# Optimization experiments

Hardware: AMD Instinct MI355X
Metric: run time of the kernel (lower is better)

Reference implementation:

```python
import jax, jax.numpy as jnp
import numpy as np

TOP_K = 2

def setup_inputs() -> dict:
    key = jax.random.key(0)
    k1, k2, k3, k4 = jax.random.split(key, 4)
    B, S, H, E, F = 2, 1024, 1024, 16, 1024
    hidden_states = jax.random.normal(k1, (B, S, H), dtype=jnp.float32)
    router_w = jax.random.normal(k2, (H, E), dtype=jnp.float32) * 0.02
    w_gate_up = jax.random.normal(k3, (E, H, 2 * F), dtype=jnp.float32) * 0.02
    w_down = jax.random.normal(k4, (E, F, H), dtype=jnp.float32) * 0.02
    return {"hidden_states": hidden_states, "router_w": router_w,
            "w_gate_up": w_gate_up, "w_down": w_down}

def reference(hidden_states, router_w, w_gate_up, w_down):
    B, S, H = hidden_states.shape
    E = router_w.shape[-1]
    flat = hidden_states.reshape(-1, H)                      # [T, H]
    T = flat.shape[0]
    # Routing: topk_then_softmax (default softmax_order)
    logits = flat @ router_w                                 # [T, E]
    top_vals, top_idx = jax.lax.top_k(logits, TOP_K)         # [T, K]
    routing_weights = jax.nn.softmax(top_vals, axis=-1)      # [T, K]
    # Scatter routing weights into a dense combine matrix [T, E]
    combine = jnp.zeros((T, E), dtype=flat.dtype)
    combine = combine.at[jnp.arange(T)[:, None], top_idx].add(routing_weights)
    # Fused expert FFN (per _FusedExpertTemplate, act_fn = SiLU-gated)
    gu = jnp.einsum('th,ehf->etf', flat, w_gate_up)          # [E, T, 2F]
    gate, up = jnp.split(gu, 2, axis=-1)
    gated = jax.nn.silu(gate) * up                           # [E, T, F]
    expert_out = jnp.einsum('etf,efh->eth', gated, w_down)   # [E, T, H]
    out = jnp.einsum('eth,te->th', expert_out, combine)      # [T, H]
    return out.reshape(B, S, H)
```

## Files before the change

kernel.cpp:

```cpp
#include <hip/hip_runtime.h>

#define T_TOK 2048
#define H_DIM 1024
#define E_NUM 16
#define F_DIM 1024
#define NKB 32

typedef unsigned short u16;
typedef unsigned int u32;
typedef short s16x8 __attribute__((ext_vector_type(8)));
typedef float f32x4 __attribute__((ext_vector_type(4)));

__device__ __forceinline__ float b2f(u16 v) { return __uint_as_float(((u32)v) << 16); }
__device__ __forceinline__ u16 f2b(float f) {
  u32 u = __float_as_uint(f);
  return (u16)((u + 0x7fffu + ((u >> 16) & 1u)) >> 16);
}

__device__ __forceinline__ void gl_lds16(const u32* g, u32* l) {
  __builtin_amdgcn_global_load_lds((const __attribute__((address_space(1))) void*)g,
                                   (__attribute__((address_space(3))) void*)l, 16, 0, 0);
}

__global__ __launch_bounds__(256) void rw_transpose_kernel(const float* __restrict__ rw,
                                                           float* __restrict__ rwT) {
  int idx = blockIdx.x * 256 + threadIdx.x;
  float v = rw[idx];
  rwT[(idx & 15) * 1024 + (idx >> 4)] = v;
}

__global__ __launch_bounds__(256) void router_kernel(const float* __restrict__ hidden,
                                                     const float* __restrict__ rwT,
                                                     int* __restrict__ counts,
                                                     int* __restrict__ routing_e,
                                                     float* __restrict__ routing_w) {
  int wv = threadIdx.x >> 6, lane = threadIdx.x & 63;
  int t = blockIdx.x * 4 + wv;
  const float* xrow = hidden + (size_t)t * H_DIM;
  float acc[E_NUM];
#pragma unroll
  for (int e = 0; e < E_NUM; ++e) acc[e] = 0.f;
  for (int j = 0; j < H_DIM / 64; ++j) {
    int h = j * 64 + lane;
    float x = xrow[h];
#pragma unroll
    for (int e = 0; e < E_NUM; ++e) acc[e] += x * rwT[e * 1024 + h];
  }
#pragma unroll
  for (int e = 0; e < E_NUM; ++e) {
    acc[e] += __shfl_xor(acc[e], 32, 64);
    acc[e] += __shfl_xor(acc[e], 16, 64);
    acc[e] += __shfl_xor(acc[e], 8, 64);
    acc[e] += __shfl_xor(acc[e], 4, 64);
    acc[e] += __shfl_xor(acc[e], 2, 64);
    acc[e] += __shfl_xor(acc[e], 1, 64);
  }
  if (lane == 0) {
    float v0 = -1e30f, v1 = -1e30f;
    int i0 = 0, i1 = 0;
#pragma unroll
    for (int e = 0; e < E_NUM; ++e) {
      float v = acc[e];
      if (v > v0) { v1 = v0; i1 = i0; v0 = v; i0 = e; }
      else if (v > v1) { v1 = v; i1 = e; }
    }
    float p0 = 1.f / (1.f + __expf(v1 - v0));
    routing_e[2 * t] = i0;
    routing_e[2 * t + 1] = i1;
    routing_w[2 * t] = p0;
    routing_w[2 * t + 1] = 1.f - p0;
    atomicAdd(&counts[i0], 1);
    atomicAdd(&counts[i1], 1);
  }
}

__global__ void scatter_kernel(const int* __restrict__ counts, int* __restrict__ offsets,
                               const int* __restrict__ routing_e, const float* __restrict__ routing_w,
                               int* __restrict__ token_of_slot, float* __restrict__ slot_w) {
  __shared__ int offs[E_NUM];
  __shared__ int cur[E_NUM];
  int tid = threadIdx.x;
  if (tid == 0) {
    int s = 0;
    for (int e = 0; e < E_NUM; ++e) { offs[e] = s; s += counts[e]; }
  }
  __syncthreads();
  if (tid < E_NUM) { offsets[tid] = offs[tid]; cur[tid] = offs[tid]; }
  __syncthreads();
  for (int i = tid; i < 2 * T_TOK; i += 256) {
    int e = routing_e[i];
    int pos = atomicAdd(&cur[e], 1);
    token_of_slot[pos] = i >> 1;
    slot_w[pos] = routing_w[i];
  }
}

__device__ __forceinline__ void split_pack(const float* __restrict__ p, uint4& hh, uint4& ll) {
  u16 h[8], l[8];
#pragma unroll
  for (int i = 0; i < 8; ++i) {
    h[i] = f2b(p[i]);
    l[i] = f2b(p[i] - b2f(h[i]));
  }
  hh.x = (u32)h[0] | ((u32)h[1] << 16);
  hh.y = (u32)h[2] | ((u32)h[3] << 16);
  hh.z = (u32)h[4] | ((u32)h[5] << 16);
  hh.w = (u32)h[6] | ((u32)h[7] << 16);
  ll.x = (u32)l[0] | ((u32)l[1] << 16);
  ll.y = (u32)l[2] | ((u32)l[3] << 16);
  ll.z = (u32)l[4] | ((u32)l[5] << 16);
  ll.w = (u32)l[6] | ((u32)l[7] << 16);
}

__global__ __launch_bounds__(256) void prep_x(const float* __restrict__ x, u16* __restrict__ xh,
                                              u16* __restrict__ xl) {
  int i = blockIdx.x * 256 + threadIdx.x;
  float4 a = ((const float4*)x)[2 * i];
  float4 b = ((const float4*)x)[2 * i + 1];
  float v[8] = {a.x, a.y, a.z, a.w, b.x, b.y, b.z, b.w};
  uint4 hh, ll;
  split_pack(v, hh, ll);
  ((uint4*)xh)[i] = hh;
  ((uint4*)xl)[i] = ll;
}

__global__ __launch_bounds__(256) void prep_w(const float* __restrict__ w, u32* __restrict__ wt,
                                              int N) {
  const int e = blockIdx.z, nbk = blockIdx.y, kb = blockIdx.x;
  const float* src = w + (size_t)e * 1024 * N + (size_t)kb * 32 * N + nbk * 128;
  u32* dst = wt + (((size_t)e * gridDim.y + nbk) * NKB + kb) * 2048;
  const int t = threadIdx.x;
  const int n = t & 127, h = t >> 7;
  const int s = ((n >> 3) ^ n) & 3;
  const float* col = src + (size_t)(16 * h) * N + n;
  float v[16];
#pragma unroll
  for (int kk = 0; kk < 16; ++kk) v[kk] = col[(size_t)kk * N];
  __align__(16) u32 wbuf[8];
#pragma unroll
  for (int j = 0; j < 8; ++j) wbuf[j] = (u32)f2b(v[2 * j]) | ((u32)f2b(v[2 * j + 1]) << 16);
  u32* row = dst + n * 16;
  *(uint4*)(row + (((2 * h) ^ s) & 3) * 4) = *(uint4*)&wbuf[0];
  *(uint4*)(row + (((2 * h + 1) ^ s) & 3) * 4) = *(uint4*)&wbuf[4];
}

__device__ __forceinline__ s16x8 read_bfrag(const u32* __restrict__ B, int n, int q) {
  return *(const s16x8*)&B[n * 16 + (((q ^ (n >> 3) ^ n) & 3) << 2)];
}

#define MFMA(a, b, c) __builtin_amdgcn_mfma_f32_16x16x32_bf16(a, b, c, 0, 0, 0)

__global__ __launch_bounds__(256, 2) void moe_gemm1(
    const u16* __restrict__ Xh, const u16* __restrict__ Xl, const u32* __restrict__ wgu_t,
    const int* __restrict__ token_of_slot, const int* __restrict__ counts,
    const int* __restrict__ offsets, u16* __restrict__ act_h, u16* __restrict__ act_l) {
  const int e = blockIdx.z;
  const int cnt = counts[e];
  const int m0 = blockIdx.y * 64;
  if (m0 >= cnt) return;
  const int off = offsets[e];
  const int xb = blockIdx.x;

  __shared__ u32 Bg[4][2048];
  __shared__ u32 Bu[4][2048];

  const int tid = threadIdx.x;
  const int lane = tid & 63;
  const int wv = tid >> 6;
  const int q = lane >> 4, ln = lane & 15;
  const int mb = (wv & 1) * 32, nb = (wv >> 1) * 64;

  const int r0 = m0 + mb + ln, r1 = r0 + 16;
  const int t0 = (r0 < cnt) ? token_of_slot[off + r0] : 0;
  const int t1 = (r1 < cnt) ? token_of_slot[off + r1] : 0;
  const u16* xh0 = Xh + (size_t)t0 * H_DIM + q * 8;
  const u16* xh1 = Xh + (size_t)t1 * H_DIM + q * 8;
  const u16* xl0 = Xl + (size_t)t0 * H_DIM + q * 8;
  const u16* xl1 = Xl + (size_t)t1 * H_DIM + q * 8;

  const u32* g_g = wgu_t + (((size_t)e * 16 + xb) * NKB) * 2048 + tid * 4;
  const u32* g_u = wgu_t + (((size_t)e * 16 + xb + 8) * NKB) * 2048 + tid * 4;

  f32x4 zero = {0.f, 0.f, 0.f, 0.f};
  f32x4 accg[2][4], accu[2][4];
#pragma unroll
  for (int i = 0; i < 2; ++i)
#pragma unroll
    for (int j = 0; j < 4; ++j) { accg[i][j] = zero; accu[i][j] = zero; }

#define G1STAGE(KBN)                                      \
  {                                                       \
    const int bix = (KBN) & 3;                            \
    const u32* sg = g_g + (size_t)(KBN) * 2048;           \
    const u32* su = g_u + (size_t)(KBN) * 2048;           \
    gl_lds16(sg, &Bg[bix][0] + wv * 256);                 \
    gl_lds16(sg + 1024, &Bg[bix][0] + 1024 + wv * 256);   \
    gl_lds16(su, &Bu[bix][0] + wv * 256);                 \
    gl_lds16(su + 1024, &Bu[bix][0] + 1024 + wv * 256);   \
  }

  s16x8 pH0, pH1, pL0, pL1, qH0, qH1, qL0, qL1;

  G1STAGE(0);
  pH0 = *(const s16x8*)(xh0);
  pH1 = *(const s16x8*)(xh1);
  pL0 = *(const s16x8*)(xl0);
  pL1 = *(const s16x8*)(xl1);
  G1STAGE(1);
  G1STAGE(2);

#define G1BODY(KB, H0, H1, L0, L1, NH0, NH1, NL0, NL1, WN, DOPF, DOST)  \
  {                                                                     \
    if (DOPF) {                                                         \
      const int ko = ((KB) + 1) * 32;                                   \
      NH0 = *(const s16x8*)(xh0 + ko);                                  \
      NH1 = *(const s16x8*)(xh1 + ko);                                  \
      NL0 = *(const s16x8*)(xl0 + ko);                                  \
      NL1 = *(const s16x8*)(xl1 + ko);                                  \
    }                                                                   \
    asm volatile("s_waitcnt vmcnt(" WN ")" ::: "memory");               \
    __builtin_amdgcn_sched_barrier(0);                                  \
    __builtin_amdgcn_s_barrier();                                       \
    __builtin_amdgcn_sched_barrier(0);                                  \
    if (DOST) G1STAGE((KB) + 3);                                        \
    const u32* Bgc = &Bg[(KB) & 3][0];                                  \
    const u32* Buc = &Bu[(KB) & 3][0];                                  \
    __builtin_amdgcn_s_setprio(1);                                      \
    _Pragma("unroll") for (int j = 0; j < 4; ++j) {                     \
      s16x8 bg = read_bfrag(Bgc, nb + j * 16 + ln, q);                  \
      s16x8 bu = read_bfrag(Buc, nb + j * 16 + ln, q);                  \
      accg[0][j] = MFMA(H0, bg, accg[0][j]);                            \
      accg[1][j] = MFMA(H1, bg, accg[1][j]);                            \
      accu[0][j] = MFMA(H0, bu, accu[0][j]);                            \
      accu[1][j] = MFMA(H1, bu, accu[1][j]);                            \
      accg[0][j] = MFMA(L0, bg, accg[0][j]);                            \
      accg[1][j] = MFMA(L1, bg, accg[1][j]);                            \
      accu[0][j] = MFMA(L0, bu, accu[0][j]);                            \
      accu[1][j] = MFMA(L1, bu, accu[1][j]);                            \
    }                                                                   \
    __builtin_amdgcn_s_setprio(0);                                      \
  }

  for (int kb = 0; kb < 28; kb += 2) {
    G1BODY(kb, pH0, pH1, pL0, pL1, qH0, qH1, qL0, qL1, "8", 1, 1);
    G1BODY(kb + 1, qH0, qH1, qL0, qL1, pH0, pH1, pL0, pL1, "8", 1, 1);
  }
  G1BODY(28, pH0, pH1, pL0, pL1, qH0, qH1, qL0, qL1, "8", 1, 1);
  G1BODY(29, qH0, qH1, qL0, qL1, pH0, pH1, pL0, pL1, "8", 1, 0);
  G1BODY(30, pH0, pH1, pL0, pL1, qH0, qH1, qL0, qL1, "4", 1, 0);
  G1BODY(31, qH0, qH1, qL0, qL1, pH0, pH1, pL0, pL1, "0", 0, 0);

  const int bcol = xb * 128 + nb + ln;
#pragma unroll
  for (int i = 0; i < 2; ++i) {
#pragma unroll
    for (int r = 0; r < 4; ++r) {
      int row = mb + i * 16 + q * 4 + r;
      if (m0 + row < cnt) {
        size_t rb = (size_t)(off + m0 + row) * F_DIM + bcol;
#pragma unroll
        for (int j = 0; j < 4; ++j) {
          float g = accg[i][j][r], u = accu[i][j][r];
          float a = g * (1.f / (1.f + __expf(-g))) * u;
          u16 h = f2b(a);
          u16 l = f2b(a - b2f(h));
          act_h[rb + j * 16] = h;
          act_l[rb + j * 16] = l;
        }
      }
    }
  }
}

__global__ __launch_bounds__(256, 3) void moe_gemm2(
    const u16* __restrict__ Ah, const u16* __restrict__ Al, const u32* __restrict__ wd_t,
    const int* __restrict__ token_of_slot, const float* __restrict__ slot_w,
    const int* __restrict__ counts, const int* __restrict__ offsets,
    float* __restrict__ out) {
  const int e = blockIdx.z;
  const int cnt = counts[e];
  const int m0 = blockIdx.y * 64;
  if (m0 >= cnt) return;
  const int off = offsets[e];
  const int xb = blockIdx.x;

  __shared__ u32 Bd[4][2048];

  const int tid = threadIdx.x;
  const int lane = tid & 63;
  const int wv = tid >> 6;
  const int q = lane >> 4, ln = lane & 15;
  const int mb = (wv & 1) * 32, nb = (wv >> 1) * 64;

  const int r0 = m0 + mb + ln, r1 = r0 + 16;
  const int s0 = off + ((r0 < cnt) ? r0 : 0);
  const int s1 = off + ((r1 < cnt) ? r1 : 0);
  const u16* ah0 = Ah + (size_t)s0 * F_DIM + q * 8;
  const u16* ah1 = Ah + (size_t)s1 * F_DIM + q * 8;
  const u16* al0 = Al + (size_t)s0 * F_DIM + q * 8;
  const u16* al1 = Al + (size_t)s1 * F_DIM + q * 8;

  const u32* g_d = wd_t + (((size_t)e * 8 + xb) * NKB) * 2048 + tid * 4;

  f32x4 zero = {0.f, 0.f, 0.f, 0.f};
  f32x4 acc[2][4];
#pragma unroll
  for (int i = 0; i < 2; ++i)
#pragma unroll
    for (int j = 0; j < 4; ++j) acc[i][j] = zero;

#define G2STAGE(KBN)                                      \
  {                                                       \
    const int bix = (KBN) & 3;                            \
    const u32* sd = g_d + (size_t)(KBN) * 2048;           \
    gl_lds16(sd, &Bd[bix][0] + wv * 256);                 \
    gl_lds16(sd + 1024, &Bd[bix][0] + 1024 + wv * 256);   \
  }

  s16x8 pH0, pH1, pL0, pL1, qH0, qH1, qL0, qL1;

  G2STAGE(0);
  pH0 = *(const s16x8*)(ah0);
  pH1 = *(const s16x8*)(ah1);
  pL0 = *(const s16x8*)(al0);
  pL1 = *(const s16x8*)(al1);
  G2STAGE(1);
  G2STAGE(2);

#define G2BODY(KB, H0, H1, L0, L1, NH0, NH1, NL0, NL1, WN, DOPF, DOST)  \
  {                                                                     \
    if (DOPF) {                                                         \
      const int ko = ((KB) + 1) * 32;                                   \
      NH0 = *(const s16x8*)(ah0 + ko);                                  \
      NH1 = *(const s16x8*)(ah1 + ko);                                  \
      NL0 = *(const s16x8*)(al0 + ko);                                  \
      NL1 = *(const s16x8*)(al1 + ko);                                  \
    }                                                                   \
    asm volatile("s_waitcnt vmcnt(" WN ")" ::: "memory");               \
    __builtin_amdgcn_sched_barrier(0);                                  \
    __builtin_amdgcn_s_barrier();                                       \
    __builtin_amdgcn_sched_barrier(0);                                  \
    if (DOST) G2STAGE((KB) + 3);                                        \
    const u32* Bdc = &Bd[(KB) & 3][0];                                  \
    __builtin_amdgcn_s_setprio(1);                                      \
    _Pragma("unroll") for (int j = 0; j < 4; ++j) {                     \
      s16x8 bf = read_bfrag(Bdc, nb + j * 16 + ln, q);                  \
      acc[0][j] = MFMA(H0, bf, acc[0][j]);                              \
      acc[1][j] = MFMA(H1, bf, acc[1][j]);                              \
      acc[0][j] = MFMA(L0, bf, acc[0][j]);                              \
      acc[1][j] = MFMA(L1, bf, acc[1][j]);                              \
    }                                                                   \
    __builtin_amdgcn_s_setprio(0);                                      \
  }

  for (int kb = 0; kb < 28; kb += 2) {
    G2BODY(kb, pH0, pH1, pL0, pL1, qH0, qH1, qL0, qL1, "6", 1, 1);
    G2BODY(kb + 1, qH0, qH1, qL0, qL1, pH0, pH1, pL0, pL1, "6", 1, 1);
  }
  G2BODY(28, pH0, pH1, pL0, pL1, qH0, qH1, qL0, qL1, "6", 1, 1);
  G2BODY(29, qH0, qH1, qL0, qL1, pH0, pH1, pL0, pL1, "6", 1, 0);
  G2BODY(30, pH0, pH1, pL0, pL1, qH0, qH1, qL0, qL1, "4", 1, 0);
  G2BODY(31, qH0, qH1, qL0, qL1, pH0, pH1, pL0, pL1, "0", 0, 0);

#pragma unroll
  for (int i = 0; i < 2; ++i) {
#pragma unroll
    for (int r = 0; r < 4; ++r) {
      int row = mb + i * 16 + q * 4 + r;
      if (m0 + row < cnt) {
        int slot = off + m0 + row;
        int tok = token_of_slot[slot];
        float wgt = slot_w[slot];
        float* orow = out + (size_t)tok * H_DIM + xb * 128 + nb + ln;
#pragma unroll
        for (int j = 0; j < 4; ++j) atomicAdd(&orow[j * 16], wgt * acc[i][j][r]);
      }
    }
  }
}

extern "C" void kernel_launch(void* const* d_in, const int* in_sizes, int n_in,
                              void* d_out, int out_size, void* d_ws, size_t ws_size,
                              hipStream_t stream) {
  const float* hidden = (const float*)d_in[0];
  const float* rw = (const float*)d_in[1];
  const float* wgu = (const float*)d_in[2];
  const float* wd = (const float*)d_in[3];
  float* out = (float*)d_out;
  char* ws = (char*)d_ws;

  int* counts = (int*)(ws);
  int* offsets = (int*)(ws + 256);
  int* routing_e = (int*)(ws + 1024);
  float* routing_w = (float*)(ws + 17408);
  int* token_of_slot = (int*)(ws + 33792);
  float* slot_w = (float*)(ws + 50176);
  float* rwT = (float*)(ws + 65536);
  u16* Xh = (u16*)(ws + 131072ull);
  u16* Xl = (u16*)(ws + 4325376ull);
  u16* act_h = (u16*)(ws + 8519680ull);
  u16* act_l = (u16*)(ws + 16908288ull);
  u32* wgu_t = (u32*)(ws + 25296896ull);
  u32* wd_t  = (u32*)(ws + 92405760ull);

  hipMemsetAsync(counts, 0, 64, stream);
  hipMemsetAsync(out, 0, (size_t)out_size * sizeof(float), stream);
  rw_transpose_kernel<<<dim3(64), dim3(256), 0, stream>>>(rw, rwT);
  router_kernel<<<dim3(T_TOK / 4), dim3(256), 0, stream>>>(hidden, rwT, counts, routing_e,
                                                           routing_w);
  scatter_kernel<<<dim3(1), dim3(256), 0, stream>>>(counts, offsets, routing_e, routing_w,
                                                    token_of_slot, slot_w);
  prep_x<<<dim3(T_TOK * H_DIM / 8 / 256), dim3(256), 0, stream>>>(hidden, Xh, Xl);
  prep_w<<<dim3(NKB, 16, E_NUM), dim3(256), 0, stream>>>(wgu, wgu_t, 2048);
  prep_w<<<dim3(NKB, 8, E_NUM), dim3(256), 0, stream>>>(wd, wd_t, 1024);
  moe_gemm1<<<dim3(8, 32, E_NUM), dim3(256), 0, stream>>>(Xh, Xl, wgu_t, token_of_slot, counts,
                                                          offsets, act_h, act_l);
  moe_gemm2<<<dim3(8, 32, E_NUM), dim3(256), 0, stream>>>(act_h, act_l, wd_t, token_of_slot,
                                                          slot_w, counts, offsets, out);
}
```

Baseline: 490.0 us.

## Fuse weight bf16 conversion into MoE GEMMs and loop over token panels

Drops the separate prep_w kernels that converted and transposed both expert weight tensors to bf16 in workspace. Each GEMM block now loads fp32 weights straight from global memory, converts them in registers and writes the swizzled tile to LDS with a double buffer. Blocks own a fixed weight column slice and loop over all token panels of an expert, so grids become 16x16 blocks of 512 threads. This avoids writing and re-reading the converted weights, but the loads become strided scalar fp32 loads, the grid is much smaller, and the async global-to-LDS loads are replaced by register staging with an extra barrier per K step.

```diff
diff --git a/kernel.cpp b/kernel.cpp
--- a/kernel.cpp
+++ b/kernel.cpp
@@ -4,7 +4,7 @@
 #define H_DIM 1024
 #define E_NUM 16
 #define F_DIM 1024
-#define NKB 32
+#define PNL 256
 
 typedef unsigned short u16;
 typedef unsigned int u32;
@@ -17,10 +17,13 @@
   return (u16)((u + 0x7fffu + ((u >> 16) & 1u)) >> 16);
 }
 
-__device__ __forceinline__ void gl_lds16(const u32* g, u32* l) {
-  __builtin_amdgcn_global_load_lds((const __attribute__((address_space(1))) void*)g,
-                                   (__attribute__((address_space(3))) void*)l, 16, 0, 0);
-}
+#define BARRIER()                                            \
+  do {                                                       \
+    asm volatile("s_waitcnt lgkmcnt(0)" ::: "memory");       \
+    __builtin_amdgcn_sched_barrier(0);                       \
+    __builtin_amdgcn_s_barrier();                            \
+    __builtin_amdgcn_sched_barrier(0);                       \
+  } while (0)
 
 __global__ __launch_bounds__(256) void rw_transpose_kernel(const float* __restrict__ rw,
                                                            float* __restrict__ rwT) {
@@ -124,256 +127,275 @@
   ((uint4*)xl)[i] = ll;
 }
 
-__global__ __launch_bounds__(256) void prep_w(const float* __restrict__ w, u32* __restrict__ wt,
-                                              int N) {
-  const int e = blockIdx.z, nbk = blockIdx.y, kb = blockIdx.x;
-  const float* src = w + (size_t)e * 1024 * N + (size_t)kb * 32 * N + nbk * 128;
-  u32* dst = wt + (((size_t)e * gridDim.y + nbk) * NKB + kb) * 2048;
-  const int t = threadIdx.x;
-  const int n = t & 127, h = t >> 7;
-  const int s = ((n >> 3) ^ n) & 3;
-  const float* col = src + (size_t)(16 * h) * N + n;
-  float v[16];
-#pragma unroll
-  for (int kk = 0; kk < 16; ++kk) v[kk] = col[(size_t)kk * N];
-  __align__(16) u32 wbuf[8];
-#pragma unroll
-  for (int j = 0; j < 8; ++j) wbuf[j] = (u32)f2b(v[2 * j]) | ((u32)f2b(v[2 * j + 1]) << 16);
-  u32* row = dst + n * 16;
-  *(uint4*)(row + (((2 * h) ^ s) & 3) * 4) = *(uint4*)&wbuf[0];
-  *(uint4*)(row + (((2 * h + 1) ^ s) & 3) * 4) = *(uint4*)&wbuf[4];
-}
-
 __device__ __forceinline__ s16x8 read_bfrag(const u32* __restrict__ B, int n, int q) {
   return *(const s16x8*)&B[n * 16 + (((q ^ (n >> 3) ^ n) & 3) << 2)];
 }
 
 #define MFMA(a, b, c) __builtin_amdgcn_mfma_f32_16x16x32_bf16(a, b, c, 0, 0, 0)
 
-__global__ __launch_bounds__(256, 2) void moe_gemm1(
-    const u16* __restrict__ Xh, const u16* __restrict__ Xl, const u32* __restrict__ wgu_t,
+
+#define WLOAD1(P, KK)                                              \
+  {                                                                \
+    const float* wp_ = wptr + (size_t)(KK) * 65536;                \
+    P##0 = wp_[0];     P##1 = wp_[2048];  P##2 = wp_[4096];        \
+    P##3 = wp_[6144];  P##4 = wp_[8192];  P##5 = wp_[10240];       \
+    P##6 = wp_[12288]; P##7 = wp_[14336];                          \
+  }
+
+#define WCVT1(P, WW)                                               \
+  {                                                                \
+    WW.x = (u32)f2b(P##0) | ((u32)f2b(P##1) << 16);                \
+    WW.y = (u32)f2b(P##2) | ((u32)f2b(P##3) << 16);                \
+    WW.z = (u32)f2b(P##4) | ((u32)f2b(P##5) << 16);                \
+    WW.w = (u32)f2b(P##6) | ((u32)f2b(P##7) << 16);                \
+  }
+
+__global__ __launch_bounds__(512, 2) void moe_gemm1(
+    const u16* __restrict__ Xh, const u16* __restrict__ Xl, const float* __restrict__ wgu,
     const int* __restrict__ token_of_slot, const int* __restrict__ counts,
     const int* __restrict__ offsets, u16* __restrict__ act_h, u16* __restrict__ act_l) {
-  const int e = blockIdx.z;
+  const int e = blockIdx.y;
   const int cnt = counts[e];
-  const int m0 = blockIdx.y * 64;
-  if (m0 >= cnt) return;
+  if (cnt == 0) return;
   const int off = offsets[e];
-  const int xb = blockIdx.x;
-
-  __shared__ u32 Bg[4][2048];
-  __shared__ u32 Bu[4][2048];
+  const int f0 = blockIdx.x * 64;
+
+  __shared__ u32 Bt[2][2048];
 
   const int tid = threadIdx.x;
   const int lane = tid & 63;
   const int wv = tid >> 6;
   const int q = lane >> 4, ln = lane & 15;
-  const int mb = (wv & 1) * 32, nb = (wv >> 1) * 64;
-
-  const int r0 = m0 + mb + ln, r1 = r0 + 16;
-  const int t0 = (r0 < cnt) ? token_of_slot[off + r0] : 0;
-  const int t1 = (r1 < cnt) ? token_of_slot[off + r1] : 0;
-  const u16* xh0 = Xh + (size_t)t0 * H_DIM + q * 8;
-  const u16* xh1 = Xh + (size_t)t1 * H_DIM + q * 8;
-  const u16* xl0 = Xl + (size_t)t0 * H_DIM + q * 8;
-  const u16* xl1 = Xl + (size_t)t1 * H_DIM + q * 8;
-
-  const u32* g_g = wgu_t + (((size_t)e * 16 + xb) * NKB) * 2048 + tid * 4;
-  const u32* g_u = wgu_t + (((size_t)e * 16 + xb + 8) * NKB) * 2048 + tid * 4;
-
-  f32x4 zero = {0.f, 0.f, 0.f, 0.f};
-  f32x4 accg[2][4], accu[2][4];
-#pragma unroll
-  for (int i = 0; i < 2; ++i)
-#pragma unroll
-    for (int j = 0; j < 4; ++j) { accg[i][j] = zero; accu[i][j] = zero; }
-
-#define G1STAGE(KBN)                                      \
-  {                                                       \
-    const int bix = (KBN) & 3;                            \
-    const u32* sg = g_g + (size_t)(KBN) * 2048;           \
-    const u32* su = g_u + (size_t)(KBN) * 2048;           \
-    gl_lds16(sg, &Bg[bix][0] + wv * 256);                 \
-    gl_lds16(sg + 1024, &Bg[bix][0] + 1024 + wv * 256);   \
-    gl_lds16(su, &Bu[bix][0] + wv * 256);                 \
-    gl_lds16(su + 1024, &Bu[bix][0] + 1024 + wv * 256);   \
-  }
-
+  const int mb = wv * 32;
+
+  const int mat = tid >> 8;
+  const int wn = ((tid >> 6) & 1) * 32 + ((tid & 63) >> 1);
+  const int wh = ((tid >> 7) & 1) * 2 + (tid & 1);
+  const float* wptr = wgu + (size_t)e * 2097152 + (size_t)(wh * 8) * 2048 + mat * 1024 + f0 + wn;
+  const int wofs = mat * 1024 + wn * 16 + (((wh ^ (wn >> 3) ^ wn) & 3) << 2);
+
+  float wa0, wa1, wa2, wa3, wa4, wa5, wa6, wa7;
+  float wb0, wb1, wb2, wb3, wb4, wb5, wb6, wb7;
   s16x8 pH0, pH1, pL0, pL1, qH0, qH1, qL0, qL1;
 
-  G1STAGE(0);
-  pH0 = *(const s16x8*)(xh0);
-  pH1 = *(const s16x8*)(xh1);
-  pL0 = *(const s16x8*)(xl0);
-  pL1 = *(const s16x8*)(xl1);
-  G1STAGE(1);
-  G1STAGE(2);
-
-#define G1BODY(KB, H0, H1, L0, L1, NH0, NH1, NL0, NL1, WN, DOPF, DOST)  \
-  {                                                                     \
-    if (DOPF) {                                                         \
-      const int ko = ((KB) + 1) * 32;                                   \
-      NH0 = *(const s16x8*)(xh0 + ko);                                  \
-      NH1 = *(const s16x8*)(xh1 + ko);                                  \
-      NL0 = *(const s16x8*)(xl0 + ko);                                  \
-      NL1 = *(const s16x8*)(xl1 + ko);                                  \
-    }                                                                   \
-    asm volatile("s_waitcnt vmcnt(" WN ")" ::: "memory");               \
-    __builtin_amdgcn_sched_barrier(0);                                  \
-    __builtin_amdgcn_s_barrier();                                       \
-    __builtin_amdgcn_sched_barrier(0);                                  \
-    if (DOST) G1STAGE((KB) + 3);                                        \
-    const u32* Bgc = &Bg[(KB) & 3][0];                                  \
-    const u32* Buc = &Bu[(KB) & 3][0];                                  \
-    __builtin_amdgcn_s_setprio(1);                                      \
-    _Pragma("unroll") for (int j = 0; j < 4; ++j) {                     \
-      s16x8 bg = read_bfrag(Bgc, nb + j * 16 + ln, q);                  \
-      s16x8 bu = read_bfrag(Buc, nb + j * 16 + ln, q);                  \
-      accg[0][j] = MFMA(H0, bg, accg[0][j]);                            \
-      accg[1][j] = MFMA(H1, bg, accg[1][j]);                            \
-      accu[0][j] = MFMA(H0, bu, accu[0][j]);                            \
-      accu[1][j] = MFMA(H1, bu, accu[1][j]);                            \
-      accg[0][j] = MFMA(L0, bg, accg[0][j]);                            \
-      accg[1][j] = MFMA(L1, bg, accg[1][j]);                            \
-      accu[0][j] = MFMA(L0, bu, accu[0][j]);                            \
-      accu[1][j] = MFMA(L1, bu, accu[1][j]);                            \
-    }                                                                   \
-    __builtin_amdgcn_s_setprio(0);                                      \
-  }
-
-  for (int kb = 0; kb < 28; kb += 2) {
-    G1BODY(kb, pH0, pH1, pL0, pL1, qH0, qH1, qL0, qL1, "8", 1, 1);
-    G1BODY(kb + 1, qH0, qH1, qL0, qL1, pH0, pH1, pL0, pL1, "8", 1, 1);
-  }
-  G1BODY(28, pH0, pH1, pL0, pL1, qH0, qH1, qL0, qL1, "8", 1, 1);
-  G1BODY(29, qH0, qH1, qL0, qL1, pH0, pH1, pL0, pL1, "8", 1, 0);
-  G1BODY(30, pH0, pH1, pL0, pL1, qH0, qH1, qL0, qL1, "4", 1, 0);
-  G1BODY(31, qH0, qH1, qL0, qL1, pH0, pH1, pL0, pL1, "0", 0, 0);
-
-  const int bcol = xb * 128 + nb + ln;
-#pragma unroll
-  for (int i = 0; i < 2; ++i) {
-#pragma unroll
-    for (int r = 0; r < 4; ++r) {
-      int row = mb + i * 16 + q * 4 + r;
-      if (m0 + row < cnt) {
-        size_t rb = (size_t)(off + m0 + row) * F_DIM + bcol;
-#pragma unroll
-        for (int j = 0; j < 4; ++j) {
-          float g = accg[i][j][r], u = accu[i][j][r];
-          float a = g * (1.f / (1.f + __expf(-g))) * u;
-          u16 h = f2b(a);
-          u16 l = f2b(a - b2f(h));
-          act_h[rb + j * 16] = h;
-          act_l[rb + j * 16] = l;
+#define G1IT(KK, PAR, WC, WN, H0, H1, L0, L1, NH0, NH1, NL0, NL1, NOTLAST, DOW) \
+  {                                                                             \
+    if (NOTLAST) {                                                              \
+      const int ko_ = ((KK) + 1) * 32;                                          \
+      NH0 = *(const s16x8*)(xh0 + ko_);                                         \
+      NH1 = *(const s16x8*)(xh1 + ko_);                                         \
+      NL0 = *(const s16x8*)(xl0 + ko_);                                         \
+      NL1 = *(const s16x8*)(xl1 + ko_);                                         \
+    }                                                                           \
+    {                                                                           \
+      const u32* Bc_ = &Bt[PAR][0];                                             \
+      __builtin_amdgcn_s_setprio(1);                                            \
+      _Pragma("unroll") for (int nf = 0; nf < 4; ++nf) {                        \
+        s16x8 bg = read_bfrag(Bc_, nf * 16 + ln, q);                            \
+        s16x8 bu = read_bfrag(Bc_ + 1024, nf * 16 + ln, q);                     \
+        accg[0][nf] = MFMA(H0, bg, accg[0][nf]);                                \
+        accg[1][nf] = MFMA(H1, bg, accg[1][nf]);                                \
+        accg[0][nf] = MFMA(L0, bg, accg[0][nf]);                                \
+        accg[1][nf] = MFMA(L1, bg, accg[1][nf]);                                \
+        accu[0][nf] = MFMA(H0, bu, accu[0][nf]);                                \
+        accu[1][nf] = MFMA(H1, bu, accu[1][nf]);                                \
+        accu[0][nf] = MFMA(L0, bu, accu[0][nf]);                                \
+        accu[1][nf] = MFMA(L1, bu, accu[1][nf]);                                \
+      }                                                                         \
+      __builtin_amdgcn_s_setprio(0);                                            \
+    }                                                                           \
+    if (NOTLAST) {                                                              \
+      uint4 ww_;                                                                \
+      WCVT1(WC, ww_);                                                           \
+      *(uint4*)&Bt[1 - (PAR)][wofs] = ww_;                                      \
+      if (DOW) WLOAD1(WN, (KK) + 2);                                            \
+      BARRIER();                                                                \
+    }                                                                           \
+  }
+
+  for (int p0 = 0; p0 < cnt; p0 += PNL) {
+    const int rr0 = p0 + mb + ln, rr1 = rr0 + 16;
+    const int t0 = (rr0 < cnt) ? token_of_slot[off + rr0] : 0;
+    const int t1 = (rr1 < cnt) ? token_of_slot[off + rr1] : 0;
+    const u16* xh0 = Xh + (size_t)t0 * H_DIM + q * 8;
+    const u16* xh1 = Xh + (size_t)t1 * H_DIM + q * 8;
+    const u16* xl0 = Xl + (size_t)t0 * H_DIM + q * 8;
+    const u16* xl1 = Xl + (size_t)t1 * H_DIM + q * 8;
+
+    f32x4 zero = {0.f, 0.f, 0.f, 0.f};
+    f32x4 accg[2][4], accu[2][4];
+#pragma unroll
+    for (int i = 0; i < 2; ++i)
+#pragma unroll
+      for (int j = 0; j < 4; ++j) { accg[i][j] = zero; accu[i][j] = zero; }
+
+    WLOAD1(wa, 0);
+    pH0 = *(const s16x8*)(xh0);
+    pH1 = *(const s16x8*)(xh1);
+    pL0 = *(const s16x8*)(xl0);
+    pL1 = *(const s16x8*)(xl1);
+    {
+      uint4 w0_;
+      WCVT1(wa, w0_);
+      *(uint4*)&Bt[0][wofs] = w0_;
+    }
+    WLOAD1(wb, 1);
+    BARRIER();
+
+    for (int kk = 0; kk < 28; kk += 2) {
+      G1IT(kk, 0, wb, wa, pH0, pH1, pL0, pL1, qH0, qH1, qL0, qL1, 1, 1);
+      G1IT(kk + 1, 1, wa, wb, qH0, qH1, qL0, qL1, pH0, pH1, pL0, pL1, 1, 1);
+    }
+    G1IT(28, 0, wb, wa, pH0, pH1, pL0, pL1, qH0, qH1, qL0, qL1, 1, 1);
+    G1IT(29, 1, wa, wb, qH0, qH1, qL0, qL1, pH0, pH1, pL0, pL1, 1, 1);
+    G1IT(30, 0, wb, wa, pH0, pH1, pL0, pL1, qH0, qH1, qL0, qL1, 1, 0);
+    G1IT(31, 1, wa, wb, qH0, qH1, qL0, qL1, pH0, pH1, pL0, pL1, 0, 0);
+
+#pragma unroll
+    for (int m = 0; m < 2; ++m) {
+#pragma unroll
+      for (int r = 0; r < 4; ++r) {
+        int rl = mb + m * 16 + q * 4 + r;
+        int sr = p0 + rl;
+        if (sr < cnt) {
+          size_t rb = (size_t)(off + sr) * F_DIM + f0 + ln;
+#pragma unroll
+          for (int nf = 0; nf < 4; ++nf) {
+            float g = accg[m][nf][r], u = accu[m][nf][r];
+            float a = g * (1.f / (1.f + __expf(-g))) * u;
+            u16 hh = f2b(a);
+            act_h[rb + nf * 16] = hh;
+            act_l[rb + nf * 16] = f2b(a - b2f(hh));
+          }
         }
       }
     }
   }
 }
 
-__global__ __launch_bounds__(256, 3) void moe_gemm2(
-    const u16* __restrict__ Ah, const u16* __restrict__ Al, const u32* __restrict__ wd_t,
+
+#define WLOAD2(P, KK)                                       \
+  {                                                         \
+    const float* wp_ = wptr2 + (size_t)(KK) * 32768;        \
+    P##0 = wp_[0];    P##1 = wp_[1024];                     \
+    P##2 = wp_[2048]; P##3 = wp_[3072];                     \
+  }
+
+#define WCVT2(P, WW)                                        \
+  {                                                         \
+    WW.x = (u32)f2b(P##0) | ((u32)f2b(P##1) << 16);         \
+    WW.y = (u32)f2b(P##2) | ((u32)f2b(P##3) << 16);         \
+  }
+
+__global__ __launch_bounds__(512, 2) void moe_gemm2(
+    const u16* __restrict__ Ah, const u16* __restrict__ Al, const float* __restrict__ wd,
     const int* __restrict__ token_of_slot, const float* __restrict__ slot_w,
     const int* __restrict__ counts, const int* __restrict__ offsets,
     float* __restrict__ out) {
-  const int e = blockIdx.z;
+  const int e = blockIdx.y;
   const int cnt = counts[e];
-  const int m0 = blockIdx.y * 64;
-  if (m0 >= cnt) return;
+  if (cnt == 0) return;
   const int off = offsets[e];
-  const int xb = blockIdx.x;
-
-  __shared__ u32 Bd[4][2048];
+  const int h0 = blockIdx.x * 64;
+
+  __shared__ u32 Bt[2][1024];
 
   const int tid = threadIdx.x;
   const int lane = tid & 63;
   const int wv = tid >> 6;
   const int q = lane >> 4, ln = lane & 15;
-  const int mb = (wv & 1) * 32, nb = (wv >> 1) * 64;
-
-  const int r0 = m0 + mb + ln, r1 = r0 + 16;
-  const int s0 = off + ((r0 < cnt) ? r0 : 0);
-  const int s1 = off + ((r1 < cnt) ? r1 : 0);
-  const u16* ah0 = Ah + (size_t)s0 * F_DIM + q * 8;
-  const u16* ah1 = Ah + (size_t)s1 * F_DIM + q * 8;
-  const u16* al0 = Al + (size_t)s0 * F_DIM + q * 8;
-  const u16* al1 = Al + (size_t)s1 * F_DIM + q * 8;
-
-  const u32* g_d = wd_t + (((size_t)e * 8 + xb) * NKB) * 2048 + tid * 4;
-
-  f32x4 zero = {0.f, 0.f, 0.f, 0.f};
-  f32x4 acc[2][4];
-#pragma unroll
-  for (int i = 0; i < 2; ++i)
-#pragma unroll
-    for (int j = 0; j < 4; ++j) acc[i][j] = zero;
-
-#define G2STAGE(KBN)                                      \
-  {                                                       \
-    const int bix = (KBN) & 3;                            \
-    const u32* sd = g_d + (size_t)(KBN) * 2048;           \
-    gl_lds16(sd, &Bd[bix][0] + wv * 256);                 \
-    gl_lds16(sd + 1024, &Bd[bix][0] + 1024 + wv * 256);   \
-  }
-
+  const int mb = wv * 32;
+
+  const int n2 = tid & 63, kpb = tid >> 6;
+  const float* wptr2 = wd + (size_t)e * 1048576 + (size_t)(kpb * 4) * 1024 + h0 + n2;
+  const int wofs2 = n2 * 16 + ((((kpb >> 1) ^ (n2 >> 3) ^ n2) & 3) << 2) + (kpb & 1) * 2;
+
+  float wa0, wa1, wa2, wa3;
+  float wb0, wb1, wb2, wb3;
   s16x8 pH0, pH1, pL0, pL1, qH0, qH1, qL0, qL1;
 
-  G2STAGE(0);
-  pH0 = *(const s16x8*)(ah0);
-  pH1 = *(const s16x8*)(ah1);
-  pL0 = *(const s16x8*)(al0);
-  pL1 = *(const s16x8*)(al1);
-  G2STAGE(1);
-  G2STAGE(2);
-
-#define G2BODY(KB, H0, H1, L0, L1, NH0, NH1, NL0, NL1, WN, DOPF, DOST)  \
-  {                                                                     \
-    if (DOPF) {                                                         \
-      const int ko = ((KB) + 1) * 32;                                   \
-      NH0 = *(const s16x8*)(ah0 + ko);                                  \
-      NH1 = *(const s16x8*)(ah1 + ko);                                  \
-      NL0 = *(const s16x8*)(al0 + ko);                                  \
-      NL1 = *(const s16x8*)(al1 + ko);                                  \
-    }                                                                   \
-    asm volatile("s_waitcnt vmcnt(" WN ")" ::: "memory");               \
-    __builtin_amdgcn_sched_barrier(0);                                  \
-    __builtin_amdgcn_s_barrier();                                       \
-    __builtin_amdgcn_sched_barrier(0);                                  \
-    if (DOST) G2STAGE((KB) + 3);                                        \
-    const u32* Bdc = &Bd[(KB) & 3][0];                                  \
-    __builtin_amdgcn_s_setprio(1);                                      \
-    _Pragma("unroll") for (int j = 0; j < 4; ++j) {                     \
-      s16x8 bf = read_bfrag(Bdc, nb + j * 16 + ln, q);                  \
-      acc[0][j] = MFMA(H0, bf, acc[0][j]);                              \
-      acc[1][j] = MFMA(H1, bf, acc[1][j]);                              \
-      acc[0][j] = MFMA(L0, bf, acc[0][j]);                              \
-      acc[1][j] = MFMA(L1, bf, acc[1][j]);                              \
-    }                                                                   \
-    __builtin_amdgcn_s_setprio(0);                                      \
-  }
-
-  for (int kb = 0; kb < 28; kb += 2) {
-    G2BODY(kb, pH0, pH1, pL0, pL1, qH0, qH1, qL0, qL1, "6", 1, 1);
-    G2BODY(kb + 1, qH0, qH1, qL0, qL1, pH0, pH1, pL0, pL1, "6", 1, 1);
-  }
-  G2BODY(28, pH0, pH1, pL0, pL1, qH0, qH1, qL0, qL1, "6", 1, 1);
-  G2BODY(29, qH0, qH1, qL0, qL1, pH0, pH1, pL0, pL1, "6", 1, 0);
-  G2BODY(30, pH0, pH1, pL0, pL1, qH0, qH1, qL0, qL1, "4", 1, 0);
-  G2BODY(31, qH0, qH1, qL0, qL1, pH0, pH1, pL0, pL1, "0", 0, 0);
-
-#pragma unroll
-  for (int i = 0; i < 2; ++i) {
-#pragma unroll
-    for (int r = 0; r < 4; ++r) {
-      int row = mb + i * 16 + q * 4 + r;
-      if (m0 + row < cnt) {
-        int slot = off + m0 + row;
-        int tok = token_of_slot[slot];
-        float wgt = slot_w[slot];
-        float* orow = out + (size_t)tok * H_DIM + xb * 128 + nb + ln;
-#pragma unroll
-        for (int j = 0; j < 4; ++j) atomicAdd(&orow[j * 16], wgt * acc[i][j][r]);
+#define G2IT(KK, PAR, WC, WN, H0, H1, L0, L1, NH0, NH1, NL0, NL1, NOTLAST, DOW) \
+  {                                                                             \
+    if (NOTLAST) {                                                              \
+      const int ko_ = ((KK) + 1) * 32;                                          \
+      NH0 = *(const s16x8*)(ah0 + ko_);                                         \
+      NH1 = *(const s16x8*)(ah1 + ko_);                                         \
+      NL0 = *(const s16x8*)(al0 + ko_);                                         \
+      NL1 = *(const s16x8*)(al1 + ko_);                                         \
+    }                                                                           \
+    {                                                                           \
+      const u32* Bc_ = &Bt[PAR][0];                                             \
+      __builtin_amdgcn_s_setprio(1);                                            \
+      _Pragma("unroll") for (int nf = 0; nf < 4; ++nf) {                        \
+        s16x8 bf = read_bfrag(Bc_, nf * 16 + ln, q);                            \
+        acc[0][nf] = MFMA(H0, bf, acc[0][nf]);                                  \
+        acc[1][nf] = MFMA(H1, bf, acc[1][nf]);                                  \
+        acc[0][nf] = MFMA(L0, bf, acc[0][nf]);                                  \
+        acc[1][nf] = MFMA(L1, bf, acc[1][nf]);                                  \
+      }                                                                         \
+      __builtin_amdgcn_s_setprio(0);                                            \
+    }                                                                           \
+    if (NOTLAST) {                                                              \
+      uint2 ww_;                                                                \
+      WCVT2(WC, ww_);                                                           \
+      *(uint2*)&Bt[1 - (PAR)][wofs2] = ww_;                                     \
+      if (DOW) WLOAD2(WN, (KK) + 2);                                            \
+      BARRIER();                                                                \
+    }                                                                           \
+  }
+
+  for (int p0 = 0; p0 < cnt; p0 += PNL) {
+    const int rr0 = p0 + mb + ln, rr1 = rr0 + 16;
+    const int s0 = off + ((rr0 < cnt) ? rr0 : 0);
+    const int s1 = off + ((rr1 < cnt) ? rr1 : 0);
+    const u16* ah0 = Ah + (size_t)s0 * F_DIM + q * 8;
+    const u16* ah1 = Ah + (size_t)s1 * F_DIM + q * 8;
+    const u16* al0 = Al + (size_t)s0 * F_DIM + q * 8;
+    const u16* al1 = Al + (size_t)s1 * F_DIM + q * 8;
+
+    f32x4 zero = {0.f, 0.f, 0.f, 0.f};
+    f32x4 acc[2][4];
+#pragma unroll
+    for (int i = 0; i < 2; ++i)
+#pragma unroll
+      for (int j = 0; j < 4; ++j) acc[i][j] = zero;
+
+    WLOAD2(wa, 0);
+    pH0 = *(const s16x8*)(ah0);
+    pH1 = *(const s16x8*)(ah1);
+    pL0 = *(const s16x8*)(al0);
+    pL1 = *(const s16x8*)(al1);
+    {
+      uint2 w0_;
+      WCVT2(wa, w0_);
+      *(uint2*)&Bt[0][wofs2] = w0_;
+    }
+    WLOAD2(wb, 1);
+    BARRIER();
+
+    for (int kk = 0; kk < 28; kk += 2) {
+      G2IT(kk, 0, wb, wa, pH0, pH1, pL0, pL1, qH0, qH1, qL0, qL1, 1, 1);
+      G2IT(kk + 1, 1, wa, wb, qH0, qH1, qL0, qL1, pH0, pH1, pL0, pL1, 1, 1);
+    }
+    G2IT(28, 0, wb, wa, pH0, pH1, pL0, pL1, qH0, qH1, qL0, qL1, 1, 1);
+    G2IT(29, 1, wa, wb, qH0, qH1, qL0, qL1, pH0, pH1, pL0, pL1, 1, 1);
+    G2IT(30, 0, wb, wa, pH0, pH1, pL0, pL1, qH0, qH1, qL0, qL1, 1, 0);
+    G2IT(31, 1, wa, wb, qH0, qH1, qL0, qL1, pH0, pH1, pL0, pL1, 0, 0);
+
+#pragma unroll
+    for (int m = 0; m < 2; ++m) {
+#pragma unroll
+      for (int r = 0; r < 4; ++r) {
+        int rl = mb + m * 16 + q * 4 + r;
+        int sr = p0 + rl;
+        if (sr < cnt) {
+          int slot = off + sr;
+          int tok = token_of_slot[slot];
+          float wgt = slot_w[slot];
+          float* orow = out + (size_t)tok * H_DIM + h0 + ln;
+#pragma unroll
+          for (int nf = 0; nf < 4; ++nf) atomicAdd(&orow[nf * 16], wgt * acc[m][nf][r]);
+        }
       }
     }
   }
@@ -400,8 +422,6 @@
   u16* Xl = (u16*)(ws + 4325376ull);
   u16* act_h = (u16*)(ws + 8519680ull);
   u16* act_l = (u16*)(ws + 16908288ull);
-  u32* wgu_t = (u32*)(ws + 25296896ull);
-  u32* wd_t  = (u32*)(ws + 92405760ull);
 
   hipMemsetAsync(counts, 0, 64, stream);
   hipMemsetAsync(out, 0, (size_t)out_size * sizeof(float), stream);
@@ -411,10 +431,8 @@
   scatter_kernel<<<dim3(1), dim3(256), 0, stream>>>(counts, offsets, routing_e, routing_w,
                                                     token_of_slot, slot_w);
   prep_x<<<dim3(T_TOK * H_DIM / 8 / 256), dim3(256), 0, stream>>>(hidden, Xh, Xl);
-  prep_w<<<dim3(NKB, 16, E_NUM), dim3(256), 0, stream>>>(wgu, wgu_t, 2048);
-  prep_w<<<dim3(NKB, 8, E_NUM), dim3(256), 0, stream>>>(wd, wd_t, 1024);
-  moe_gemm1<<<dim3(8, 32, E_NUM), dim3(256), 0, stream>>>(Xh, Xl, wgu_t, token_of_slot, counts,
-                                                          offsets, act_h, act_l);
-  moe_gemm2<<<dim3(8, 32, E_NUM), dim3(256), 0, stream>>>(act_h, act_l, wd_t, token_of_slot,
-                                                          slot_w, counts, offsets, out);
-}
+  moe_gemm1<<<dim3(16, 16), dim3(512), 0, stream>>>(Xh, Xl, wgu, token_of_slot, counts,
+                                                    offsets, act_h, act_l);
+  moe_gemm2<<<dim3(16, 16), dim3(512), 0, stream>>>(act_h, act_l, wd, token_of_slot,
+                                                    slot_w, counts, offsets, out);
+}
```

New measurement: 425.6 us. -13.1%, faster.
